# Optimization experiments

Hardware: AMD Instinct MI355X
Metric: run time of the kernel (lower is better)

The kernel has to match this reference:

```python
import jax, jax.numpy as jnp
import numpy as np

N = 50000
E = 800000
IN_DIM, HID, OUT_DIM, HEADS = 256, 128, 64, 4


def _segment_sum(vals, ids, n):
    return jax.ops.segment_sum(vals, ids, num_segments=n)


def gcn_conv(x, src, dst, W, b, n):
    # PyG GCNConv: add self loops, symmetric normalization, aggregate at dst
    xw = x @ W  # [N, HID]
    loop = jnp.arange(n, dtype=src.dtype)
    srcA = jnp.concatenate([src, loop])
    dstA = jnp.concatenate([dst, loop])
    deg = _segment_sum(jnp.ones_like(srcA, dtype=xw.dtype), dstA, n)
    dinv = jnp.where(deg > 0, jax.lax.rsqrt(deg), 0.0)
    norm = dinv[srcA] * dinv[dstA]  # [E+N]
    msg = xw[srcA] * norm[:, None]  # [E+N, HID] -- dominant memory traffic
    return _segment_sum(msg, dstA, n) + b


def layer_norm(h, gamma, beta, eps=1e-5):
    mu = jnp.mean(h, axis=-1, keepdims=True)
    var = jnp.mean(jnp.square(h - mu), axis=-1, keepdims=True)
    return (h - mu) * jax.lax.rsqrt(var + eps) * gamma + beta


def gat_conv(x, src, dst, W, att_src, att_dst, b, n):
    # PyG GATConv (concat=True), self-loops added, eval mode (no dropout)
    xw = (x @ W).reshape(n, HEADS, HID)  # [N, H, C]
    a_s = jnp.sum(xw * att_src, axis=-1)  # [N, H]
    a_d = jnp.sum(xw * att_dst, axis=-1)  # [N, H]
    loop = jnp.arange(n, dtype=src.dtype)
    srcA = jnp.concatenate([src, loop])
    dstA = jnp.concatenate([dst, loop])
    e = jax.nn.leaky_relu(a_s[srcA] + a_d[dstA], 0.2)  # [E+N, H]
    m = jax.ops.segment_max(e, dstA, num_segments=n)  # [N, H]
    ex = jnp.exp(e - m[dstA])
    denom = _segment_sum(ex, dstA, n)  # [N, H] (>=1 entry per node via self loop)
    alpha = ex / denom[dstA]  # [E+N, H]
    msg = xw[srcA] * alpha[:, :, None]  # [E+N, H, C]
    out = _segment_sum(msg, dstA, n)  # [N, H, C]
    return out.reshape(n, HEADS * HID) + b


def setup_inputs() -> dict:
    key = jax.random.key(0)
    ks = jax.random.split(key, 16)
    x = jax.random.normal(ks[0], (N, IN_DIM), dtype=jnp.float32)
    edge_index = jax.random.randint(ks[1], (2, E), 0, N, dtype=jnp.int64)
    s = lambda k, shape, fan: jax.random.normal(k, shape, jnp.float32) / np.sqrt(fan)
    return {
        "x": x,
        "edge_index": edge_index,
        "Win": s(ks[2], (IN_DIM, HID), IN_DIM),
        "bin_": jnp.zeros((HID,), jnp.float32),
        "Wg1": s(ks[3], (HID, HID), HID),
        "bg1": jnp.zeros((HID,), jnp.float32),
        "g1_gamma": jnp.ones((HID,), jnp.float32),
        "g1_beta": jnp.zeros((HID,), jnp.float32),
        "Wg2": s(ks[4], (HID, HID), HID),
        "bg2": jnp.zeros((HID,), jnp.float32),
        "g2_gamma": jnp.ones((HID,), jnp.float32),
        "g2_beta": jnp.zeros((HID,), jnp.float32),
        "Wgat": s(ks[5], (HID, HEADS * HID), HID),
        "att_src": s(ks[6], (HEADS, HID), HID),
        "att_dst": s(ks[7], (HEADS, HID), HID),
        "bgat": jnp.zeros((HEADS * HID,), jnp.float32),
        "Watt_out": s(ks[8], (HEADS * HID, HID), HEADS * HID),
        "batt_out": jnp.zeros((HID,), jnp.float32),
        "Wout": s(ks[9], (HID, OUT_DIM), HID),
        "bout": jnp.zeros((OUT_DIM,), jnp.float32),
    }


def reference(x, edge_index, Win, bin_, Wg1, bg1, g1_gamma, g1_beta,
              Wg2, bg2, g2_gamma, g2_beta, Wgat, att_src, att_dst, bgat,
              Watt_out, batt_out, Wout, bout):
    src, dst = edge_index[0], edge_index[1]
    n = x.shape[0]
    # input projection (dropout = identity in eval)
    h0 = jax.nn.relu(x @ Win + bin_)
    # NOTE: original zip truncates -> only 2 of the 3 GCN layers execute.
    # layer 0 (i==0: no residual)
    h = gcn_conv(h0, src, dst, Wg1, bg1, n)
    h = jax.nn.relu(layer_norm(h, g1_gamma, g1_beta))
    x1 = h
    # layer 1 (i==1: residual)
    h = gcn_conv(x1, src, dst, Wg2, bg2, n)
    h = jax.nn.relu(layer_norm(h, g2_gamma, g2_beta))
    x2 = x1 + h
    # GAT attention block
    a = gat_conv(x2, src, dst, Wgat, att_src, att_dst, bgat, n)
    a = jax.nn.relu(a @ Watt_out + batt_out)
    # output projection
    return a @ Wout + bout
```

## Files before the change

### kernel.cpp

```cpp
#include <hip/hip_runtime.h>
#include <hip/hip_bf16.h>
#include <cstddef>
#include <cstdint>

#define TPB 256
#define HID 128
#define GATD 512
#define HEADS 4

typedef __attribute__((ext_vector_type(8))) short bf16x8;
typedef __attribute__((ext_vector_type(4))) float f32x4;

__device__ __forceinline__ float lrelu02(float x) { return x > 0.0f ? x : 0.2f * x; }

__device__ __forceinline__ unsigned short f2bf_rn(float f) {
  uint32_t u = __float_as_uint(f);
  u += 0x7fff + ((u >> 16) & 1);
  return (unsigned short)(u >> 16);
}
__device__ __forceinline__ float bf2f(unsigned short h) {
  return __uint_as_float(((uint32_t)h) << 16);
}
__device__ __forceinline__ float bflo(uint32_t u) { return __uint_as_float(u << 16); }
__device__ __forceinline__ float bfhi(uint32_t u) { return __uint_as_float(u & 0xffff0000u); }

__global__ void k_zero(int* __restrict__ p, int n) {
  int i = blockIdx.x * blockDim.x + threadIdx.x;
  if (i < n) p[i] = 0;
}

__global__ void k_hist(const int* __restrict__ dst, int* __restrict__ cnt, int E) {
  int i = blockIdx.x * blockDim.x + threadIdx.x;
  if (i < E) atomicAdd(&cnt[dst[i]], 1);
}

__global__ __launch_bounds__(256) void k_scan_blk(const int* __restrict__ cnt,
                                                  int* __restrict__ rowp,
                                                  int* __restrict__ bsum,
                                                  float* __restrict__ dinv, int n) {
  __shared__ int wsum[4];
  const int tid = threadIdx.x, lane = tid & 63, wid = tid >> 6;
  const int base = blockIdx.x * 1024 + tid * 4;
  int v[4];
#pragma unroll
  for (int q = 0; q < 4; ++q) {
    int idx = base + q;
    v[q] = (idx < n) ? cnt[idx] : 0;
    if (idx < n) dinv[idx] = rsqrtf((float)(v[q] + 1));
  }
  int s = v[0] + v[1] + v[2] + v[3];
  int sc = s;
#pragma unroll
  for (int off = 1; off < 64; off <<= 1) {
    int t = __shfl_up(sc, off);
    if (lane >= off) sc += t;
  }
  if (lane == 63) wsum[wid] = sc;
  __syncthreads();
  int woff = 0;
#pragma unroll
  for (int w = 0; w < 4; ++w)
    if (w < wid) woff += wsum[w];
  int run = woff + sc - s;
#pragma unroll
  for (int q = 0; q < 4; ++q) {
    int idx = base + q;
    if (idx < n) rowp[idx] = run;
    run += v[q];
  }
  if (tid == 255) bsum[blockIdx.x] = woff + sc;
}

__global__ __launch_bounds__(256) void k_scan_top(int* __restrict__ bsum, int nb) {
  __shared__ int sm[256];
  const int tid = threadIdx.x;
  int v = (tid < nb) ? bsum[tid] : 0;
  sm[tid] = v;
  __syncthreads();
  for (int off = 1; off < 256; off <<= 1) {
    int t = (tid >= off) ? sm[tid - off] : 0;
    __syncthreads();
    sm[tid] += t;
    __syncthreads();
  }
  int incl = sm[tid];
  if (tid < nb) bsum[tid] = incl - v;
  if (tid == nb - 1) bsum[nb] = incl;
}

__global__ void k_scan_add(int* __restrict__ rowp, const int* __restrict__ bsum,
                           int n, int nb) {
  int i = blockIdx.x * blockDim.x + threadIdx.x;
  if (i < n) rowp[i] += bsum[i >> 10];
  if (i == 0) rowp[n] = bsum[nb];
}

__global__ void k_fill(const int* __restrict__ src, const int* __restrict__ dst,
                       const int* __restrict__ rowp, int* __restrict__ cur,
                       int* __restrict__ colsrc, int E) {
  int i = blockIdx.x * blockDim.x + threadIdx.x;
  if (i < E) {
    int d = dst[i];
    int pos = rowp[d] + atomicAdd(&cur[d], 1);
    colsrc[pos] = src[i];
  }
}

__global__ void k_splitw_all(const float* __restrict__ Win, const float* __restrict__ Wg1,
                             const float* __restrict__ Wg2, const float* __restrict__ Wout,
                             unsigned short* __restrict__ WinTh, unsigned short* __restrict__ WinTl,
                             unsigned short* __restrict__ Wg1Th, unsigned short* __restrict__ Wg1Tl,
                             unsigned short* __restrict__ Wg2Th, unsigned short* __restrict__ Wg2Tl,
                             unsigned short* __restrict__ WoutTh, unsigned short* __restrict__ WoutTl) {
  int t = blockIdx.x * blockDim.x + threadIdx.x;
  const float* W;
  unsigned short *H, *L;
  int K, NC, r;
  if (t < 32768)      { W = Win;  H = WinTh;  L = WinTl;  K = 256; NC = 128; r = t; }
  else if (t < 49152) { W = Wg1;  H = Wg1Th;  L = Wg1Tl;  K = 128; NC = 128; r = t - 32768; }
  else if (t < 65536) { W = Wg2;  H = Wg2Th;  L = Wg2Tl;  K = 128; NC = 128; r = t - 49152; }
  else if (t < 73728) { W = Wout; H = WoutTh; L = WoutTl; K = 128; NC = 64;  r = t - 65536; }
  else return;
  int k = r / NC, n2 = r % NC;
  float v = W[r];
  unsigned short h = f2bf_rn(v);
  H[(size_t)n2 * K + k] = h;
  L[(size_t)n2 * K + k] = f2bf_rn(v - bf2f(h));
}

__global__ __launch_bounds__(256) void k_prep(const float* __restrict__ Wgat,
                                              const float* __restrict__ att_src,
                                              const float* __restrict__ att_dst,
                                              const float* __restrict__ Wao,
                                              const float* __restrict__ bgat,
                                              const float* __restrict__ bao,
                                              float* __restrict__ waT,
                                              unsigned short* __restrict__ V2Th,
                                              unsigned short* __restrict__ V2Tl,
                                              float* __restrict__ cb) {
  int t = blockIdx.x * blockDim.x + threadIdx.x;
  if (t < 1024) {
    int p = t >> 7, k = t & 127;
    int h = p & 3;
    const float* av = (p < 4 ? att_src : att_dst) + h * HID;
    const float* wrow = Wgat + (size_t)k * GATD + h * HID;
    float s = 0.f;
#pragma unroll 4
    for (int c = 0; c < HID; ++c) s = fmaf(wrow[c], av[c], s);
    waT[t] = s;
  } else if (t < 1024 + 65536) {
    int r = t - 1024;
    int j = r >> 7, k = r & 127;
    int c = j >> 2, h = j & 3;
    const float* wg = Wgat + (size_t)k * GATD + h * HID;
    const float* wa = Wao + (size_t)(h * HID) * HID + c;
    float s = 0.f;
#pragma unroll 4
    for (int d = 0; d < HID; ++d) s = fmaf(wg[d], wa[(size_t)d * HID], s);
    unsigned short hi = f2bf_rn(s);
    V2Th[(size_t)c * GATD + k * 4 + h] = hi;
    V2Tl[(size_t)c * GATD + k * 4 + h] = f2bf_rn(s - bf2f(hi));
  } else if (t < 1024 + 65536 + 128) {
    int c = t - 1024 - 65536;
    float s = bao[c];
    for (int d = 0; d < GATD; ++d) s = fmaf(bgat[d], Wao[(size_t)d * HID + c], s);
    cb[c] = s;
  }
}

template <int KTOT, int KC, int NCB, bool RELU, bool BIAS, int OUTM, int AMODE>
__global__ __launch_bounds__(256) void k_gemm6(
    const void* __restrict__ Av,
    const unsigned short* __restrict__ BhT, const unsigned short* __restrict__ BlT,
    const float* __restrict__ bias, void* __restrict__ Cv, int M, int NC) {
  constexpr int NSUB = KC / 32;
  constexpr int NCHUNK = KTOT / KC;
  constexpr int NCF = NCB / 16;
  constexpr int UNITS = NSUB * 2 * 4 * NCB;
  __shared__ alignas(16) unsigned short Bs[NSUB][2][4][NCB][8];
  const int tid = threadIdx.x, lane = tid & 63, wid = tid >> 6;
  const int m0 = blockIdx.x * 64;
  const int n0 = blockIdx.y * NCB;
  const int fr = lane & 15, g = lane >> 4;
  const int arow = m0 + wid * 16 + fr;
  const bool aok = arow < M;
  const size_t abase = (size_t)arow * KTOT;

  f32x4 acc[NCF];
#pragma unroll
  for (int cf = 0; cf < NCF; ++cf) acc[cf] = (f32x4){0.f, 0.f, 0.f, 0.f};

  for (int c = 0; c < NCHUNK; ++c) {
    const int c0 = c * KC;
    if (c > 0) __syncthreads();
#pragma unroll
    for (int it = 0; it < UNITS / 256; ++it) {
      const int u = tid + it * 256;
      const int n = u % NCB;
      int rest = u / NCB;
      const int kg = rest & 3;
      rest >>= 2;
      const int p = rest & 1;
      const int sub = rest >> 1;
      const unsigned short* sp =
          (p ? BlT : BhT) + (size_t)(n0 + n) * KTOT + c0 + sub * 32 + kg * 8;
      *(uint4*)&Bs[sub][p][kg][n][0] = *(const uint4*)sp;
    }
    __syncthreads();
#pragma unroll
    for (int sub = 0; sub < NSUB; ++sub) {
      const int kb = c0 + sub * 32 + g * 8;
      bf16x8 a = {};
      if (aok) {
        if (AMODE == 0) {
          a = *(const bf16x8*)((const unsigned short*)Av + abase + kb);
        } else {
          const float* Af = (const float*)Av + abase + kb;
          float4 q0 = *(const float4*)Af;
          float4 q1 = *(const float4*)(Af + 4);
          float av[8] = {q0.x, q0.y, q0.z, q0.w, q1.x, q1.y, q1.z, q1.w};
          union { bf16x8 v; uint32_t u4[4]; } Hu;
#pragma unroll
          for (int q = 0; q < 4; ++q) {
            Hu.u4[q] = (uint32_t)f2bf_rn(av[2 * q]) | ((uint32_t)f2bf_rn(av[2 * q + 1]) << 16);
          }
          a = Hu.v;
        }
      }
#pragma unroll
      for (int cf = 0; cf < NCF; ++cf) {
        bf16x8 b_h = *(const bf16x8*)&Bs[sub][0][g][cf * 16 + fr][0];
        bf16x8 b_l = *(const bf16x8*)&Bs[sub][1][g][cf * 16 + fr][0];
        acc[cf] = __builtin_amdgcn_mfma_f32_16x16x32_bf16(a, b_h, acc[cf], 0, 0, 0);
        acc[cf] = __builtin_amdgcn_mfma_f32_16x16x32_bf16(a, b_l, acc[cf], 0, 0, 0);
      }
    }
  }
#pragma unroll
  for (int cf = 0; cf < NCF; ++cf) {
    const int col = n0 + cf * 16 + fr;
    const float bv = BIAS ? bias[col] : 0.f;
#pragma unroll
    for (int r = 0; r < 4; ++r) {
      const int grow = m0 + wid * 16 + g * 4 + r;
      if (grow < M) {
        float v = acc[cf][r] + bv;
        if (RELU) v = fmaxf(v, 0.f);
        const size_t idx = (size_t)grow * NC + col;
        if (OUTM == 0) ((float*)Cv)[idx] = v;
        else ((unsigned short*)Cv)[idx] = f2bf_rn(v);
      }
    }
  }
}

template <bool L2>
__global__ __launch_bounds__(256) void k_gcn_agg(
    const unsigned short* __restrict__ xwb, const float* __restrict__ dinv,
    const int* __restrict__ rowp, const int* __restrict__ colsrc,
    const float* __restrict__ bias, const float* __restrict__ gamma,
    const float* __restrict__ beta,
    const unsigned short* __restrict__ resb,
    unsigned short* __restrict__ ob,
    const float* __restrict__ waT, float* __restrict__ a_s, float* __restrict__ a_d,
    int n) {
  __shared__ float w[8][HID];
  if (L2) {
    for (int t = threadIdx.x; t < 8 * HID; t += 256) ((float*)w)[t] = waT[t];
    __syncthreads();
  }
  const int lane = threadIdx.x & 63;
  const int i = blockIdx.x * 4 + (threadIdx.x >> 6);
  if (i >= n) return;
  const float di = dinv[i];
  const int c = lane * 2;
  uint32_t v0 = *(const uint32_t*)(xwb + (size_t)i * HID + c);
  float a0 = bflo(v0) * di * di, a1 = bfhi(v0) * di * di;
  float b0 = 0.f, b1 = 0.f;
  const int e0 = rowp[i], e1 = rowp[i + 1];
  int j = e0;
  for (; j + 7 < e1; j += 8) {
    int ss[8];
    float ww[8];
    uint32_t uu[8];
#pragma unroll
    for (int q = 0; q < 8; ++q) ss[q] = colsrc[j + q];
#pragma unroll
    for (int q = 0; q < 8; ++q) ww[q] = dinv[ss[q]] * di;
#pragma unroll
    for (int q = 0; q < 8; ++q) uu[q] = *(const uint32_t*)(xwb + (size_t)ss[q] * HID + c);
#pragma unroll
    for (int q = 0; q < 8; ++q) {
      if (q & 1) {
        b0 = fmaf(bflo(uu[q]), ww[q], b0);
        b1 = fmaf(bfhi(uu[q]), ww[q], b1);
      } else {
        a0 = fmaf(bflo(uu[q]), ww[q], a0);
        a1 = fmaf(bfhi(uu[q]), ww[q], a1);
      }
    }
  }
  for (; j < e1; ++j) {
    int s0 = colsrc[j];
    float w0 = dinv[s0] * di;
    uint32_t u0 = *(const uint32_t*)(xwb + (size_t)s0 * HID + c);
    a0 = fmaf(bflo(u0), w0, a0);
    a1 = fmaf(bfhi(u0), w0, a1);
  }
  a0 += b0;
  a1 += b1;
  a0 += bias[c];
  a1 += bias[c + 1];
  float s1 = a0 + a1, s2 = a0 * a0 + a1 * a1;
#pragma unroll
  for (int m = 32; m >= 1; m >>= 1) {
    s1 += __shfl_xor(s1, m);
    s2 += __shfl_xor(s2, m);
  }
  float mu = s1 * (1.0f / HID);
  float var = s2 * (1.0f / HID) - mu * mu;
  float rstd = rsqrtf(var + 1e-5f);
  float y0 = fmaxf((a0 - mu) * rstd * gamma[c] + beta[c], 0.0f);
  float y1 = fmaxf((a1 - mu) * rstd * gamma[c + 1] + beta[c + 1], 0.0f);
  if (L2) {
    uint32_t rb = *(const uint32_t*)(resb + (size_t)i * HID + c);
    y0 += bflo(rb);
    y1 += bfhi(rb);
  }
  *(uint32_t*)(ob + (size_t)i * HID + c) =
      (uint32_t)f2bf_rn(y0) | ((uint32_t)f2bf_rn(y1) << 16);
  if (L2) {
    float p[8];
#pragma unroll
    for (int h = 0; h < 8; ++h) p[h] = y0 * w[h][c] + y1 * w[h][c + 1];
#pragma unroll
    for (int m = 32; m >= 1; m >>= 1) {
#pragma unroll
      for (int h = 0; h < 8; ++h) p[h] += __shfl_xor(p[h], m);
    }
    if (lane == 0) {
      a_s[i * 4 + 0] = p[0]; a_s[i * 4 + 1] = p[1];
      a_s[i * 4 + 2] = p[2]; a_s[i * 4 + 3] = p[3];
      a_d[i * 4 + 0] = p[4]; a_d[i * 4 + 1] = p[5];
      a_d[i * 4 + 2] = p[6]; a_d[i * 4 + 3] = p[7];
    }
  }
}

__global__ __launch_bounds__(256) void k_gat_agg4(const unsigned short* __restrict__ x2b,
                                                  const float* __restrict__ a_s,
                                                  const float* __restrict__ a_d,
                                                  const int* __restrict__ rowp,
                                                  const int* __restrict__ colsrc,
                                                  unsigned short* __restrict__ ub,
                                                  int n) {
  __shared__ float4 albuf[4][64];
  __shared__ int sbuf[4][64];
  const int lane = threadIdx.x & 63;
  const int wid = threadIdx.x >> 6;
  const int i = blockIdx.x * 4 + wid;
  if (i >= n) return;
  const float4 adv = *(const float4*)(a_d + i * 4);
  const float4 asv = *(const float4*)(a_s + i * 4);
  float es0 = lrelu02(asv.x + adv.x);
  float es1 = lrelu02(asv.y + adv.y);
  float es2 = lrelu02(asv.z + adv.z);
  float es3 = lrelu02(asv.w + adv.w);
  const int e0 = rowp[i], e1 = rowp[i + 1];
  float m0 = es0, m1 = es1, m2 = es2, m3 = es3;
  for (int j = e0 + lane; j < e1; j += 64) {
    int s = colsrc[j];
    const float4 av = *(const float4*)(a_s + s * 4);
    m0 = fmaxf(m0, lrelu02(av.x + adv.x));
    m1 = fmaxf(m1, lrelu02(av.y + adv.y));
    m2 = fmaxf(m2, lrelu02(av.z + adv.z));
    m3 = fmaxf(m3, lrelu02(av.w + adv.w));
  }
#pragma unroll
  for (int m = 32; m >= 1; m >>= 1) {
    m0 = fmaxf(m0, __shfl_xor(m0, m));
    m1 = fmaxf(m1, __shfl_xor(m1, m));
    m2 = fmaxf(m2, __shfl_xor(m2, m));
    m3 = fmaxf(m3, __shfl_xor(m3, m));
  }
  float d0 = 0.f, d1 = 0.f, d2 = 0.f, d3 = 0.f;
  for (int j = e0 + lane; j < e1; j += 64) {
    int s = colsrc[j];
    const float4 av = *(const float4*)(a_s + s * 4);
    d0 += __expf(lrelu02(av.x + adv.x) - m0);
    d1 += __expf(lrelu02(av.y + adv.y) - m1);
    d2 += __expf(lrelu02(av.z + adv.z) - m2);
    d3 += __expf(lrelu02(av.w + adv.w) - m3);
  }
#pragma unroll
  for (int m = 32; m >= 1; m >>= 1) {
    d0 += __shfl_xor(d0, m);
    d1 += __shfl_xor(d1, m);
    d2 += __shfl_xor(d2, m);
    d3 += __shfl_xor(d3, m);
  }
  d0 += __expf(es0 - m0);
  d1 += __expf(es1 - m1);
  d2 += __expf(es2 - m2);
  d3 += __expf(es3 - m3);
  const float inv0 = 1.0f / d0, inv1 = 1.0f / d1, inv2 = 1.0f / d2, inv3 = 1.0f / d3;
  const float4 asf = make_float4(__expf(es0 - m0) * inv0, __expf(es1 - m1) * inv1,
                                 __expf(es2 - m2) * inv2, __expf(es3 - m3) * inv3);
  const int c0 = lane * 2;
  uint32_t sv = *(const uint32_t*)(x2b + (size_t)i * HID + c0);
  float x0 = bflo(sv), x1 = bfhi(sv);
  float4 A0 = make_float4(x0 * asf.x, x0 * asf.y, x0 * asf.z, x0 * asf.w);
  float4 A1 = make_float4(x1 * asf.x, x1 * asf.y, x1 * asf.z, x1 * asf.w);
  for (int b = e0; b < e1; b += 64) {
    int j = b + lane;
    if (j < e1) {
      int s = colsrc[j];
      const float4 av = *(const float4*)(a_s + s * 4);
      albuf[wid][lane] = make_float4(__expf(lrelu02(av.x + adv.x) - m0) * inv0,
                                     __expf(lrelu02(av.y + adv.y) - m1) * inv1,
                                     __expf(lrelu02(av.z + adv.z) - m2) * inv2,
                                     __expf(lrelu02(av.w + adv.w) - m3) * inv3);
      sbuf[wid][lane] = s;
    }
    asm volatile("s_waitcnt lgkmcnt(0)" ::: "memory");
    const int cnt = min(64, e1 - b);
    for (int t = 0; t < cnt; ++t) {
      float4 a4 = albuf[wid][t];
      int s = sbuf[wid][t];
      uint32_t wv = *(const uint32_t*)(x2b + (size_t)s * HID + c0);
      float w0 = bflo(wv), w1 = bfhi(wv);
      A0.x = fmaf(w0, a4.x, A0.x); A0.y = fmaf(w0, a4.y, A0.y);
      A0.z = fmaf(w0, a4.z, A0.z); A0.w = fmaf(w0, a4.w, A0.w);
      A1.x = fmaf(w1, a4.x, A1.x); A1.y = fmaf(w1, a4.y, A1.y);
      A1.z = fmaf(w1, a4.z, A1.z); A1.w = fmaf(w1, a4.w, A1.w);
    }
  }
  uint4 o;
  o.x = (uint32_t)f2bf_rn(A0.x) | ((uint32_t)f2bf_rn(A0.y) << 16);
  o.y = (uint32_t)f2bf_rn(A0.z) | ((uint32_t)f2bf_rn(A0.w) << 16);
  o.z = (uint32_t)f2bf_rn(A1.x) | ((uint32_t)f2bf_rn(A1.y) << 16);
  o.w = (uint32_t)f2bf_rn(A1.z) | ((uint32_t)f2bf_rn(A1.w) << 16);
  *(uint4*)(ub + (size_t)i * GATD + lane * 8) = o;
}

extern "C" void kernel_launch(void* const* d_in, const int* in_sizes, int n_in,
                              void* d_out, int out_size, void* d_ws, size_t ws_size,
                              hipStream_t stream) {
  const float* x = (const float*)d_in[0];
  const int* ei = (const int*)d_in[1];
  const float* Win = (const float*)d_in[2];
  const float* bin = (const float*)d_in[3];
  const float* Wg1 = (const float*)d_in[4];
  const float* bg1 = (const float*)d_in[5];
  const float* g1g = (const float*)d_in[6];
  const float* g1b = (const float*)d_in[7];
  const float* Wg2 = (const float*)d_in[8];
  const float* bg2 = (const float*)d_in[9];
  const float* g2g = (const float*)d_in[10];
  const float* g2b = (const float*)d_in[11];
  const float* Wgat = (const float*)d_in[12];
  const float* att_s = (const float*)d_in[13];
  const float* att_d = (const float*)d_in[14];
  const float* bgat = (const float*)d_in[15];
  const float* Wao = (const float*)d_in[16];
  const float* bao = (const float*)d_in[17];
  const float* Wout = (const float*)d_in[18];
  const float* bout = (const float*)d_in[19];

  const int N = in_sizes[0] / 256;
  const int E = in_sizes[1] / 2;
  const int* src = ei;
  const int* dst = ei + E;

  char* base = (char*)d_ws;
  size_t off = 0;
  unsigned short* h0b = (unsigned short*)(base + off); off += (size_t)N * HID * 2;
  unsigned short* x1b = (unsigned short*)(base + off); off += (size_t)N * HID * 2;
  unsigned short* xwb = (unsigned short*)(base + off); off += (size_t)N * HID * 2;
  unsigned short* x2b = (unsigned short*)(base + off); off += (size_t)N * HID * 2;
  unsigned short* ub = (unsigned short*)(base + off); off += (size_t)N * GATD * 2;
  unsigned short* attb = h0b;
  float* dinv = (float*)(base + off);                 off += (size_t)N * 4;
  float* a_s = (float*)(base + off);                  off += (size_t)N * 16;
  float* a_d = (float*)(base + off);                  off += (size_t)N * 16;
  float* waT = (float*)(base + off);                  off += 4096;
  float* cb = (float*)(base + off);                   off += 512;
  unsigned short *WinTh, *WinTl, *Wg1Th, *Wg1Tl, *Wg2Th, *Wg2Tl, *V2Th, *V2Tl;
  unsigned short *WoutTh, *WoutTl;
  WinTh = (unsigned short*)(base + off); off += 256 * 128 * 2;
  WinTl = (unsigned short*)(base + off); off += 256 * 128 * 2;
  Wg1Th = (unsigned short*)(base + off); off += 128 * 128 * 2;
  Wg1Tl = (unsigned short*)(base + off); off += 128 * 128 * 2;
  Wg2Th = (unsigned short*)(base + off); off += 128 * 128 * 2;
  Wg2Tl = (unsigned short*)(base + off); off += 128 * 128 * 2;
  V2Th = (unsigned short*)(base + off);  off += 512 * 128 * 2;
  V2Tl = (unsigned short*)(base + off);  off += 512 * 128 * 2;
  WoutTh = (unsigned short*)(base + off); off += 128 * 64 * 2;
  WoutTl = (unsigned short*)(base + off); off += 128 * 64 * 2;
  int* rowp = (int*)(base + off);   off += (size_t)(N + 1) * 4;
  int* colsrc = (int*)(base + off); off += (size_t)E * 4;
  const int nb2 = (N + 1023) / 1024;
  int* bsum = (int*)(base + off);   off += (size_t)(nb2 + 2) * 4;
  int* cnt = (int*)ub;
  int* cur = cnt + N;

  const int eb = (E + TPB - 1) / TPB;
  const int zbk = (2 * N + TPB - 1) / TPB;
  const int ab = (N + 3) / 4;
  const int gm = (N + 63) / 64;

  k_zero<<<zbk, TPB, 0, stream>>>(cnt, 2 * N);
  k_hist<<<eb, TPB, 0, stream>>>(dst, cnt, E);
  k_scan_blk<<<nb2, 256, 0, stream>>>(cnt, rowp, bsum, dinv, N);
  k_scan_top<<<1, 256, 0, stream>>>(bsum, nb2);
  k_scan_add<<<(N + 255) / 256, 256, 0, stream>>>(rowp, bsum, N, nb2);
  k_fill<<<eb, TPB, 0, stream>>>(src, dst, rowp, cur, colsrc, E);
  k_prep<<<(1024 + 65536 + 128 + 255) / 256, 256, 0, stream>>>(
      Wgat, att_s, att_d, Wao, bgat, bao, waT, V2Th, V2Tl, cb);
  k_splitw_all<<<(73728 + 255) / 256, 256, 0, stream>>>(
      Win, Wg1, Wg2, Wout, WinTh, WinTl, Wg1Th, Wg1Tl, Wg2Th, Wg2Tl, WoutTh, WoutTl);

  k_gemm6<256, 64, 128, true, true, 1, 1><<<dim3(gm, 1), 256, 0, stream>>>(
      x, WinTh, WinTl, bin, h0b, N, 128);
  k_gemm6<128, 64, 128, false, false, 1, 0><<<dim3(gm, 1), 256, 0, stream>>>(
      h0b, Wg1Th, Wg1Tl, nullptr, xwb, N, 128);
  k_gcn_agg<false><<<ab, 256, 0, stream>>>(xwb, dinv, rowp, colsrc, bg1, g1g, g1b,
                                           nullptr, x1b, nullptr, nullptr, nullptr, N);
  k_gemm6<128, 64, 128, false, false, 1, 0><<<dim3(gm, 1), 256, 0, stream>>>(
      x1b, Wg2Th, Wg2Tl, nullptr, xwb, N, 128);
  k_gcn_agg<true><<<ab, 256, 0, stream>>>(xwb, dinv, rowp, colsrc, bg2, g2g, g2b,
                                          x1b, x2b, waT, a_s, a_d, N);
  k_gat_agg4<<<ab, 256, 0, stream>>>(x2b, a_s, a_d, rowp, colsrc, ub, N);
  k_gemm6<512, 64, 128, true, true, 1, 0><<<dim3(gm, 1), 256, 0, stream>>>(
      ub, V2Th, V2Tl, cb, attb, N, 128);
  k_gemm6<128, 128, 64, false, true, 0, 0><<<dim3(gm, 1), 256, 0, stream>>>(
      attb, WoutTh, WoutTl, bout, (float*)d_out, N, 64);
}
```

Before: 419.1 us.

## Fold GCN source normalization into GEMM epilogue and fuse GAT softmax denominator pass

The GEMM that produces xw now multiplies each output row by dinv, so the GCN aggregation only sums pre-scaled neighbor rows and applies the destination dinv once, removing a per-edge dinv gather and multiply. In the GAT aggregation, the separate pass that computed the softmax denominator is dropped: the unnormalized exponentials are accumulated alongside the weighted sum and divided by the reduced denominator at the end. This removes one full edge sweep with its a_s gathers and exps per node. The trade-off is slightly different rounding, because the dinv-scaled values are stored in bf16 and normalization is deferred to the end.

```diff
diff --git a/kernel.cpp b/kernel.cpp
--- a/kernel.cpp
+++ b/kernel.cpp
@@ -168,11 +168,12 @@
   }
 }
 
-template <int KTOT, int KC, int NCB, bool RELU, bool BIAS, int OUTM, int AMODE>
+template <int KTOT, int KC, int NCB, bool RELU, bool BIAS, int OUTM, int AMODE, bool SCALE>
 __global__ __launch_bounds__(256) void k_gemm6(
     const void* __restrict__ Av,
     const unsigned short* __restrict__ BhT, const unsigned short* __restrict__ BlT,
-    const float* __restrict__ bias, void* __restrict__ Cv, int M, int NC) {
+    const float* __restrict__ bias, const float* __restrict__ rowsc,
+    void* __restrict__ Cv, int M, int NC) {
   constexpr int NSUB = KC / 32;
   constexpr int NCHUNK = KTOT / KC;
   constexpr int NCF = NCB / 16;
@@ -246,6 +247,7 @@
       if (grow < M) {
         float v = acc[cf][r] + bv;
         if (RELU) v = fmaxf(v, 0.f);
+        if (SCALE) v *= rowsc[grow];
         const size_t idx = (size_t)grow * NC + col;
         if (OUTM == 0) ((float*)Cv)[idx] = v;
         else ((unsigned short*)Cv)[idx] = f2bf_rn(v);
@@ -256,7 +258,7 @@
 
 template <bool L2>
 __global__ __launch_bounds__(256) void k_gcn_agg(
-    const unsigned short* __restrict__ xwb, const float* __restrict__ dinv,
+    const unsigned short* __restrict__ xws, const float* __restrict__ dinv,
     const int* __restrict__ rowp, const int* __restrict__ colsrc,
     const float* __restrict__ bias, const float* __restrict__ gamma,
     const float* __restrict__ beta,
@@ -274,43 +276,37 @@
   if (i >= n) return;
   const float di = dinv[i];
   const int c = lane * 2;
-  uint32_t v0 = *(const uint32_t*)(xwb + (size_t)i * HID + c);
-  float a0 = bflo(v0) * di * di, a1 = bfhi(v0) * di * di;
+  uint32_t v0 = *(const uint32_t*)(xws + (size_t)i * HID + c);
+  float a0 = bflo(v0), a1 = bfhi(v0);
   float b0 = 0.f, b1 = 0.f;
   const int e0 = rowp[i], e1 = rowp[i + 1];
   int j = e0;
   for (; j + 7 < e1; j += 8) {
     int ss[8];
-    float ww[8];
     uint32_t uu[8];
 #pragma unroll
     for (int q = 0; q < 8; ++q) ss[q] = colsrc[j + q];
 #pragma unroll
-    for (int q = 0; q < 8; ++q) ww[q] = dinv[ss[q]] * di;
-#pragma unroll
-    for (int q = 0; q < 8; ++q) uu[q] = *(const uint32_t*)(xwb + (size_t)ss[q] * HID + c);
+    for (int q = 0; q < 8; ++q) uu[q] = *(const uint32_t*)(xws + (size_t)ss[q] * HID + c);
 #pragma unroll
     for (int q = 0; q < 8; ++q) {
       if (q & 1) {
-        b0 = fmaf(bflo(uu[q]), ww[q], b0);
-        b1 = fmaf(bfhi(uu[q]), ww[q], b1);
+        b0 += bflo(uu[q]);
+        b1 += bfhi(uu[q]);
       } else {
-        a0 = fmaf(bflo(uu[q]), ww[q], a0);
-        a1 = fmaf(bfhi(uu[q]), ww[q], a1);
+        a0 += bflo(uu[q]);
+        a1 += bfhi(uu[q]);
       }
     }
   }
   for (; j < e1; ++j) {
     int s0 = colsrc[j];
-    float w0 = dinv[s0] * di;
-    uint32_t u0 = *(const uint32_t*)(xwb + (size_t)s0 * HID + c);
-    a0 = fmaf(bflo(u0), w0, a0);
-    a1 = fmaf(bfhi(u0), w0, a1);
-  }
-  a0 += b0;
-  a1 += b1;
-  a0 += bias[c];
-  a1 += bias[c + 1];
+    uint32_t u0 = *(const uint32_t*)(xws + (size_t)s0 * HID + c);
+    a0 += bflo(u0);
+    a1 += bfhi(u0);
+  }
+  a0 = (a0 + b0) * di + bias[c];
+  a1 = (a1 + b1) * di + bias[c + 1];
   float s1 = a0 + a1, s2 = a0 * a0 + a1 * a1;
 #pragma unroll
   for (int m = 32; m >= 1; m >>= 1) {
@@ -383,43 +379,25 @@
     m2 = fmaxf(m2, __shfl_xor(m2, m));
     m3 = fmaxf(m3, __shfl_xor(m3, m));
   }
-  float d0 = 0.f, d1 = 0.f, d2 = 0.f, d3 = 0.f;
-  for (int j = e0 + lane; j < e1; j += 64) {
-    int s = colsrc[j];
-    const float4 av = *(const float4*)(a_s + s * 4);
-    d0 += __expf(lrelu02(av.x + adv.x) - m0);
-    d1 += __expf(lrelu02(av.y + adv.y) - m1);
-    d2 += __expf(lrelu02(av.z + adv.z) - m2);
-    d3 += __expf(lrelu02(av.w + adv.w) - m3);
-  }
-#pragma unroll
-  for (int m = 32; m >= 1; m >>= 1) {
-    d0 += __shfl_xor(d0, m);
-    d1 += __shfl_xor(d1, m);
-    d2 += __shfl_xor(d2, m);
-    d3 += __shfl_xor(d3, m);
-  }
-  d0 += __expf(es0 - m0);
-  d1 += __expf(es1 - m1);
-  d2 += __expf(es2 - m2);
-  d3 += __expf(es3 - m3);
-  const float inv0 = 1.0f / d0, inv1 = 1.0f / d1, inv2 = 1.0f / d2, inv3 = 1.0f / d3;
-  const float4 asf = make_float4(__expf(es0 - m0) * inv0, __expf(es1 - m1) * inv1,
-                                 __expf(es2 - m2) * inv2, __expf(es3 - m3) * inv3);
+  const float e_self0 = __expf(es0 - m0), e_self1 = __expf(es1 - m1);
+  const float e_self2 = __expf(es2 - m2), e_self3 = __expf(es3 - m3);
   const int c0 = lane * 2;
   uint32_t sv = *(const uint32_t*)(x2b + (size_t)i * HID + c0);
   float x0 = bflo(sv), x1 = bfhi(sv);
-  float4 A0 = make_float4(x0 * asf.x, x0 * asf.y, x0 * asf.z, x0 * asf.w);
-  float4 A1 = make_float4(x1 * asf.x, x1 * asf.y, x1 * asf.z, x1 * asf.w);
+  float4 A0 = make_float4(x0 * e_self0, x0 * e_self1, x0 * e_self2, x0 * e_self3);
+  float4 A1 = make_float4(x1 * e_self0, x1 * e_self1, x1 * e_self2, x1 * e_self3);
+  float dp0 = 0.f, dp1 = 0.f, dp2 = 0.f, dp3 = 0.f;
   for (int b = e0; b < e1; b += 64) {
     int j = b + lane;
     if (j < e1) {
       int s = colsrc[j];
       const float4 av = *(const float4*)(a_s + s * 4);
-      albuf[wid][lane] = make_float4(__expf(lrelu02(av.x + adv.x) - m0) * inv0,
-                                     __expf(lrelu02(av.y + adv.y) - m1) * inv1,
-                                     __expf(lrelu02(av.z + adv.z) - m2) * inv2,
-                                     __expf(lrelu02(av.w + adv.w) - m3) * inv3);
+      float e0v = __expf(lrelu02(av.x + adv.x) - m0);
+      float e1v = __expf(lrelu02(av.y + adv.y) - m1);
+      float e2v = __expf(lrelu02(av.z + adv.z) - m2);
+      float e3v = __expf(lrelu02(av.w + adv.w) - m3);
+      dp0 += e0v; dp1 += e1v; dp2 += e2v; dp3 += e3v;
+      albuf[wid][lane] = make_float4(e0v, e1v, e2v, e3v);
       sbuf[wid][lane] = s;
     }
     asm volatile("s_waitcnt lgkmcnt(0)" ::: "memory");
@@ -435,6 +413,17 @@
       A1.z = fmaf(w1, a4.z, A1.z); A1.w = fmaf(w1, a4.w, A1.w);
     }
   }
+#pragma unroll
+  for (int m = 32; m >= 1; m >>= 1) {
+    dp0 += __shfl_xor(dp0, m);
+    dp1 += __shfl_xor(dp1, m);
+    dp2 += __shfl_xor(dp2, m);
+    dp3 += __shfl_xor(dp3, m);
+  }
+  const float inv0 = 1.0f / (dp0 + e_self0), inv1 = 1.0f / (dp1 + e_self1);
+  const float inv2 = 1.0f / (dp2 + e_self2), inv3 = 1.0f / (dp3 + e_self3);
+  A0.x *= inv0; A0.y *= inv1; A0.z *= inv2; A0.w *= inv3;
+  A1.x *= inv0; A1.y *= inv1; A1.z *= inv2; A1.w *= inv3;
   uint4 o;
   o.x = (uint32_t)f2bf_rn(A0.x) | ((uint32_t)f2bf_rn(A0.y) << 16);
   o.y = (uint32_t)f2bf_rn(A0.z) | ((uint32_t)f2bf_rn(A0.w) << 16);
@@ -520,19 +509,19 @@
   k_splitw_all<<<(73728 + 255) / 256, 256, 0, stream>>>(
       Win, Wg1, Wg2, Wout, WinTh, WinTl, Wg1Th, Wg1Tl, Wg2Th, Wg2Tl, WoutTh, WoutTl);
 
-  k_gemm6<256, 64, 128, true, true, 1, 1><<<dim3(gm, 1), 256, 0, stream>>>(
-      x, WinTh, WinTl, bin, h0b, N, 128);
-  k_gemm6<128, 64, 128, false, false, 1, 0><<<dim3(gm, 1), 256, 0, stream>>>(
-      h0b, Wg1Th, Wg1Tl, nullptr, xwb, N, 128);
+  k_gemm6<256, 64, 128, true, true, 1, 1, false><<<dim3(gm, 1), 256, 0, stream>>>(
+      x, WinTh, WinTl, bin, nullptr, h0b, N, 128);
+  k_gemm6<128, 64, 128, false, false, 1, 0, true><<<dim3(gm, 1), 256, 0, stream>>>(
+      h0b, Wg1Th, Wg1Tl, nullptr, dinv, xwb, N, 128);
   k_gcn_agg<false><<<ab, 256, 0, stream>>>(xwb, dinv, rowp, colsrc, bg1, g1g, g1b,
                                            nullptr, x1b, nullptr, nullptr, nullptr, N);
-  k_gemm6<128, 64, 128, false, false, 1, 0><<<dim3(gm, 1), 256, 0, stream>>>(
-      x1b, Wg2Th, Wg2Tl, nullptr, xwb, N, 128);
+  k_gemm6<128, 64, 128, false, false, 1, 0, true><<<dim3(gm, 1), 256, 0, stream>>>(
+      x1b, Wg2Th, Wg2Tl, nullptr, dinv, xwb, N, 128);
   k_gcn_agg<true><<<ab, 256, 0, stream>>>(xwb, dinv, rowp, colsrc, bg2, g2g, g2b,
                                           x1b, x2b, waT, a_s, a_d, N);
   k_gat_agg4<<<ab, 256, 0, stream>>>(x2b, a_s, a_d, rowp, colsrc, ub, N);
-  k_gemm6<512, 64, 128, true, true, 1, 0><<<dim3(gm, 1), 256, 0, stream>>>(
-      ub, V2Th, V2Tl, cb, attb, N, 128);
-  k_gemm6<128, 128, 64, false, true, 0, 0><<<dim3(gm, 1), 256, 0, stream>>>(
-      attb, WoutTh, WoutTl, bout, (float*)d_out, N, 64);
-}
+  k_gemm6<512, 64, 128, true, true, 1, 0, false><<<dim3(gm, 1), 256, 0, stream>>>(
+      ub, V2Th, V2Tl, cb, nullptr, attb, N, 128);
+  k_gemm6<128, 128, 64, false, true, 0, 0, false><<<dim3(gm, 1), 256, 0, stream>>>(
+      attb, WoutTh, WoutTl, bout, nullptr, (float*)d_out, N, 64);
+}
```

Measured after the change: 420.3 us. About the same (+0.3%).
